# Performance work log

Hardware: AMD Instinct MI355X
Metric: run time of the kernel (lower is better)

## Reference

```python
import jax, jax.numpy as jnp
import numpy as np
from jax import lax

B, T, N, D, M, K, H = 16, 96, 256, 128, 1196, 8, 4
HD = D // H  # head dim = 32
TAU_TIME = 2.0


def setup_inputs() -> dict:
    key = jax.random.key(0)
    ks = jax.random.split(key, 12)
    w = lambda k, shp: jax.random.normal(k, shp, jnp.float32) * 0.05
    return {
        "x_scalar": jax.random.normal(ks[0], (B, T, N), jnp.float32),
        "season_q": jax.random.randint(ks[1], (B,), 0, 4),
        "year_q": 2010.0 + 10.0 * jax.random.uniform(ks[2], (B,), jnp.float32),
        "dw_w": w(ks[3], (N, 1, 12)),          # depthwise Conv1d weight (out=N, in/groups=1, k=12)
        "dw_b": jnp.zeros((N,), jnp.float32),
        "pw_w": w(ks[4], (N * D, N)),          # pointwise Conv1d weight (out=N*D, in=N), k=1 squeezed
        "pw_b": jnp.zeros((N * D,), jnp.float32),
        "ln_g": jnp.ones((D,), jnp.float32),
        "ln_b": jnp.zeros((D,), jnp.float32),
        "memory_bank": jax.random.normal(ks[5], (M, N, D), jnp.float32),
        "memory_seasons": jax.random.randint(ks[6], (M,), 0, 4),
        "memory_years": 2010.0 + 10.0 * jax.random.uniform(ks[7], (M,), jnp.float32),
        "in_proj_w": w(ks[8], (3 * D, D)),     # MHA packed q/k/v projection
        "in_proj_b": jnp.zeros((3 * D,), jnp.float32),
        "out_proj_w": w(ks[9], (D, D)),
        "out_proj_b": jnp.zeros((D,), jnp.float32),
        "proj_w": w(ks[10], (D, D)),
        "proj_b": jnp.zeros((D,), jnp.float32),
    }


def _layernorm(x, g, b, eps=1e-5):
    mu = jnp.mean(x, axis=-1, keepdims=True)
    var = jnp.mean((x - mu) ** 2, axis=-1, keepdims=True)
    return (x - mu) * lax.rsqrt(var + eps) * g + b


def _l2norm(x, eps=1e-12):
    n = jnp.sqrt(jnp.sum(x * x, axis=-1, keepdims=True))
    return x / jnp.maximum(n, eps)


def _forward(x_scalar, season_q, year_q, dw_w, dw_b, pw_w, pw_b, ln_g, ln_b,
             memory_bank, memory_seasons, memory_years,
             in_proj_w, in_proj_b, out_proj_w, out_proj_b, proj_w, proj_b):
    b, t, n = x_scalar.shape
    d = ln_g.shape[0]
    m = memory_bank.shape[0]

    # --- TemporalEncoder ---
    x = jnp.transpose(x_scalar, (0, 2, 1))  # (b, n, t): permute(0,2,3,1).reshape with d_input=1
    x = lax.conv_general_dilated(
        x, dw_w, window_strides=(1,), padding=[(6, 6)],
        dimension_numbers=("NCH", "OIH", "NCH"), feature_group_count=n)
    x = jax.nn.gelu(x + dw_b[:, None], approximate=False)      # (b, n, t+1)
    x = jnp.einsum("bct,oc->bot", x, pw_w) + pw_b[:, None]     # pointwise 1x1 conv -> (b, n*d, t+1)
    x = jax.nn.gelu(x, approximate=False)
    x = jnp.mean(x, axis=-1).reshape(b, n, d)                  # adaptive avg pool to 1
    q = _layernorm(x, ln_g, ln_b)                              # (b, n, d)

    # --- retrieve ---
    qf = _l2norm(q.reshape(b, n * d))
    memf = _l2norm(memory_bank.reshape(m, n * d))
    sim = qf @ memf.T                                          # (b, m)
    smask = (season_q[:, None] == memory_seasons[None, :]).astype(sim.dtype)
    sim = sim * smask + (1.0 - smask) * (-10000.0)
    dy = jnp.abs(year_q[:, None] - memory_years[None, :])
    diversity = 1.0 - jnp.exp(-dy / max(TAU_TIME, 1e-4))
    sim = sim * (0.5 + 0.5 * diversity)
    _, idx = lax.top_k(sim, K)                                 # (b, K)
    retrieved = memory_bank[idx]                               # (b, K, n, d)

    # --- cross attention: query (b*n, 1, d) vs kv (b*n, K, d) ---
    Wq, Wk, Wv = in_proj_w[:d], in_proj_w[d:2 * d], in_proj_w[2 * d:]
    bq, bk, bv = in_proj_b[:d], in_proj_b[d:2 * d], in_proj_b[2 * d:]
    kv = jnp.transpose(retrieved, (0, 2, 1, 3))                # (b, n, K, d)
    qp = (jnp.einsum("bnd,ed->bne", q, Wq) + bq).reshape(b, n, H, HD)
    kp = (jnp.einsum("bnkd,ed->bnke", kv, Wk) + bk).reshape(b, n, K, H, HD)
    vp = (jnp.einsum("bnkd,ed->bnke", kv, Wv) + bv).reshape(b, n, K, H, HD)
    scores = jnp.einsum("bnhe,bnkhe->bnhk", qp, kp) / np.sqrt(HD)
    attn = jax.nn.softmax(scores, axis=-1)
    ctx = jnp.einsum("bnhk,bnkhe->bnhe", attn, vp).reshape(b, n, d)
    out = jnp.einsum("bnd,ed->bne", ctx, out_proj_w) + out_proj_b
    out = jnp.einsum("bnd,ed->bne", out, proj_w) + proj_b
    return out, q


def reference(x_scalar, season_q, year_q, dw_w, dw_b, pw_w, pw_b, ln_g, ln_b,
              memory_bank, memory_seasons, memory_years,
              in_proj_w, in_proj_b, out_proj_w, out_proj_b, proj_w, proj_b):
    return _forward(x_scalar, season_q, year_q, dw_w, dw_b, pw_w, pw_b, ln_g, ln_b,
                    memory_bank, memory_seasons, memory_years,
                    in_proj_w, in_proj_b, out_proj_w, out_proj_b, proj_w, proj_b)
```

## Files before the change

kernel.cpp:

```cpp
#include <hip/hip_runtime.h>

typedef _Float16 f16x8 __attribute__((ext_vector_type(8)));
typedef _Float16 f16x4 __attribute__((ext_vector_type(4)));
typedef float    f32x4 __attribute__((ext_vector_type(4)));

__device__ __forceinline__ float gelu_f(float x) {
    float z  = 0.70710678118654752440f * x;
    float az = fabsf(z);
    float t  = 1.0f / fmaf(0.3275911f, az, 1.0f);
    float e  = __expf(-az * az);
    float p  = t * fmaf(t, fmaf(t, fmaf(t, fmaf(t, 1.061405429f, -1.453152027f),
                                        1.421413741f), -0.284496736f), 0.254829592f);
    float er = fmaf(-p, e, 1.0f);
    float s  = (z < 0.0f) ? -er : er;
    return 0.5f * x * (1.0f + s);
}

__device__ __forceinline__ void gload16(const void* g, void* l) {
    __builtin_amdgcn_global_load_lds(
        (const __attribute__((address_space(1))) unsigned int*)g,
        (__attribute__((address_space(3))) unsigned int*)l, 16, 0, 0);
}

__global__ void conv_kernel(const float* __restrict__ xs, const float* __restrict__ dww,
                            const float* __restrict__ dwb, _Float16* __restrict__ Gt)
{
    int b = blockIdx.x, t = blockIdx.y, n = threadIdx.x;
    float g = 0.f;
    if (t < 97) {
        float y = 0.f;
        #pragma unroll
        for (int j = 0; j < 12; ++j) {
            int tt = t + j - 6;
            if (tt >= 0 && tt < 96)
                y += dww[n*12 + j] * xs[((size_t)b*96 + tt)*256 + n];
        }
        g = gelu_f(y + dwb[n]);
    }
    Gt[((size_t)b*128 + t)*256 + n] = (_Float16)g;
}

__global__ void cvt_pw_kernel(const float* __restrict__ src, _Float16* __restrict__ dst,
                              const float* __restrict__ ipw, const float* __restrict__ opw,
                              const float* __restrict__ pjw, _Float16* __restrict__ wAll,
                              float* __restrict__ zp)
{
    int bid = blockIdx.x, tid = threadIdx.x;
    if (bid < 8192) {
        size_t i = ((size_t)bid*256 + tid) * 4;
        float4 v = *(const float4*)&src[i];
        f16x4 o; o[0] = (_Float16)v.x; o[1] = (_Float16)v.y; o[2] = (_Float16)v.z; o[3] = (_Float16)v.w;
        *(f16x4*)&dst[i] = o;
    } else if (bid < 8512) {
        int i = (bid - 8192)*256 + tid;
        float v = (i < 49152) ? ipw[i] : (i < 65536 ? opw[i - 49152] : pjw[i - 65536]);
        wAll[i] = (_Float16)v;
    } else {
        int i = (bid - 8512)*256 + tid;
        if (i < 5087) {
            float4 z = {0.f, 0.f, 0.f, 0.f};
            *(float4*)&zp[i*4] = z;
        }
    }
}

__global__ __launch_bounds__(256) void pw_kernel(const _Float16* __restrict__ W,
                                                 const _Float16* __restrict__ Gt,
                                                 const float* __restrict__ pwb,
                                                 float* __restrict__ xmean)
{
    __shared__ __align__(16) _Float16 As[2][128][32];
    __shared__ __align__(16) _Float16 Bs[2][128][32];

    int x = blockIdx.x;
    int xcd = x & 7, ii = x >> 3;
    int ob = xcd * 32 + (ii >> 4);
    int b  = ii & 15;
    const _Float16* Arow = W  + (size_t)ob * 128 * 256;
    const _Float16* Brow = Gt + (size_t)b  * 128 * 256;

    int tid = threadIdx.x, w = tid >> 6, l = tid & 63, lr = l & 15, lk = l >> 4;
    int wr = w >> 1, wc = w & 1;
    int rsw = (lr >> 1) & 3;

    f32x4 acc[4][4];
    #pragma unroll
    for (int i = 0; i < 4; ++i)
        #pragma unroll
        for (int j = 0; j < 4; ++j)
            acc[i][j] = f32x4{0.f, 0.f, 0.f, 0.f};

    auto stage = [&](int buf, int k0) {
        #pragma unroll
        for (int j = 0; j < 2; ++j) {
            int chunk = tid + j*256;
            int row = chunk >> 2;
            int co  = (chunk & 3) * 8;
            int cos = ((chunk & 3) ^ ((chunk >> 3) & 3)) * 8;
            gload16(&Arow[row*256 + k0 + cos], &As[buf][row][co]);
            gload16(&Brow[row*256 + k0 + cos], &Bs[buf][row][co]);
        }
    };

    stage(0, 0);
    __syncthreads();
    for (int ks = 0; ks < 8; ++ks) {
        int cur = ks & 1;
        if (ks < 7) stage(cur ^ 1, (ks + 1) * 32);
        f16x8 a[4], bb[4];
        #pragma unroll
        for (int i = 0; i < 4; ++i)
            a[i]  = *(const f16x8*)&As[cur][wr*64 + i*16 + lr][(lk ^ rsw)*8];
        #pragma unroll
        for (int j = 0; j < 4; ++j)
            if (wc == 0 || j < 3)
                bb[j] = *(const f16x8*)&Bs[cur][wc*64 + j*16 + lr][(lk ^ rsw)*8];
        #pragma unroll
        for (int i = 0; i < 4; ++i)
            #pragma unroll
            for (int j = 0; j < 4; ++j)
                if (wc == 0 || j < 3)
                    acc[i][j] = __builtin_amdgcn_mfma_f32_16x16x32_f16(bb[j], a[i], acc[i][j], 0, 0, 0);
        __syncthreads();
    }

    float (*red)[2] = reinterpret_cast<float(*)[2]>(&As[0][0][0]);
    #pragma unroll
    for (int i = 0; i < 4; ++i) {
        int og = ob*128 + wr*64 + i*16 + lr;
        float pbv = pwb[og];
        float s = 0.f;
        if (wc == 0) {
            #pragma unroll
            for (int j = 0; j < 4; ++j)
                #pragma unroll
                for (int r = 0; r < 4; ++r)
                    s += gelu_f(acc[i][j][r] + pbv);
        } else {
            #pragma unroll
            for (int j = 0; j < 2; ++j)
                #pragma unroll
                for (int r = 0; r < 4; ++r)
                    s += gelu_f(acc[i][j][r] + pbv);
            if (lk == 0) s += gelu_f(acc[i][2][0] + pbv);
        }
        s += __shfl_xor(s, 16, 64);
        s += __shfl_xor(s, 32, 64);
        if (lk == 0) red[wr*64 + i*16 + lr][wc] = s;
    }
    __syncthreads();
    if (tid < 128) {
        float v = (red[tid][0] + red[tid][1]) * (1.f / 97.f);
        xmean[(size_t)b*32768 + ob*128 + tid] = v;
    }
}

__global__ void ln_kernel(const float* __restrict__ xm, const float* __restrict__ g,
                          const float* __restrict__ bta, float* __restrict__ qout,
                          _Float16* __restrict__ qh, _Float16* __restrict__ qlo,
                          float* __restrict__ qss)
{
    int bn = blockIdx.x, lane = threadIdx.x;
    float x0 = xm[(size_t)bn*128 + lane];
    float x1 = xm[(size_t)bn*128 + 64 + lane];
    float s = x0 + x1;
    #pragma unroll
    for (int m = 1; m < 64; m <<= 1) s += __shfl_xor(s, m, 64);
    float mu = s * (1.f/128.f);
    float d0 = x0 - mu, d1 = x1 - mu;
    float v = d0*d0 + d1*d1;
    #pragma unroll
    for (int m = 1; m < 64; m <<= 1) v += __shfl_xor(v, m, 64);
    float rs = 1.0f / sqrtf(v * (1.f/128.f) + 1e-5f);
    float q0 = d0*rs*g[lane]    + bta[lane];
    float q1 = d1*rs*g[64+lane] + bta[64+lane];
    qout[(size_t)bn*128 + lane]      = q0;
    qout[(size_t)bn*128 + 64 + lane] = q1;
    _Float16 h0 = (_Float16)q0, h1 = (_Float16)q1;
    qh[(size_t)bn*128 + lane]      = h0;
    qh[(size_t)bn*128 + 64 + lane] = h1;
    qlo[(size_t)bn*128 + lane]      = (_Float16)(q0 - (float)h0);
    qlo[(size_t)bn*128 + 64 + lane] = (_Float16)(q1 - (float)h1);
    float ss = q0*q0 + q1*q1;
    #pragma unroll
    for (int m = 1; m < 64; m <<= 1) ss += __shfl_xor(ss, m, 64);
    if (lane == 0) atomicAdd(&qss[bn >> 8], ss);
}

__global__ __launch_bounds__(256) void simgemm_kernel(const _Float16* __restrict__ qhi,
                                                      const _Float16* __restrict__ qlo,
                                                      const float* __restrict__ mem,
                                                      float* __restrict__ dotp,
                                                      float* __restrict__ mn2)
{
    __shared__ __align__(16) float Ms[2][16][256];
    __shared__ f32x4 redls[4][64];
    __shared__ float redn[4][16];

    int tid = threadIdx.x, w = tid >> 6, l = tid & 63, lr = l & 15, lk = l >> 4;
    int m0 = blockIdx.y * 16;
    int kwin = blockIdx.x * 1024;
    int rowm = m0 + lr;

    auto stage = [&](int buf, int sw) {
        #pragma unroll
        for (int j = 0; j < 4; ++j) {
            int r = w*4 + j;
            int rowg = m0 + r; if (rowg > 1195) rowg = 1195;
            const float* src = mem + (size_t)rowg*32768 + kwin + sw*256 + (l ^ (r & 7))*4;
            gload16(src, &Ms[buf][r][0]);
        }
    };

    f32x4 acc_a = {0.f,0.f,0.f,0.f}, acc_b = {0.f,0.f,0.f,0.f};
    float nacc = 0.f;

    stage(0, 0);
    __syncthreads();
    for (int sw = 0; sw < 4; ++sw) {
        int cur = sw & 1;
        if (sw < 3) stage(cur ^ 1, sw + 1);
        #pragma unroll
        for (int cc = 0; cc < 2; ++cc) {
            int kl = w*64 + cc*32;
            int s0 = (kl + lk*8) >> 2;
            float4 v0 = *(const float4*)&Ms[cur][lr][(s0       ^ (lr & 7))*4];
            float4 v1 = *(const float4*)&Ms[cur][lr][((s0 + 1) ^ (lr & 7))*4];
            int kg = kwin + sw*256 + kl + lk*8;
            f16x8 ah = *(const f16x8*)&qhi[(size_t)lr*32768 + kg];
            f16x8 al = *(const f16x8*)&qlo[(size_t)lr*32768 + kg];
            float e0 = v0.x, e1 = v0.y, e2 = v0.z, e3 = v0.w;
            float e4 = v1.x, e5 = v1.y, e6 = v1.z, e7 = v1.w;
            f16x8 bh;
            bh[0]=(_Float16)e0; bh[1]=(_Float16)e1; bh[2]=(_Float16)e2; bh[3]=(_Float16)e3;
            bh[4]=(_Float16)e4; bh[5]=(_Float16)e5; bh[6]=(_Float16)e6; bh[7]=(_Float16)e7;
            nacc = fmaf(e0,e0, fmaf(e1,e1, fmaf(e2,e2, fmaf(e3,e3, nacc))));
            nacc = fmaf(e4,e4, fmaf(e5,e5, fmaf(e6,e6, fmaf(e7,e7, nacc))));
            acc_a = __builtin_amdgcn_mfma_f32_16x16x32_f16(ah, bh, acc_a, 0, 0, 0);
            acc_b = __builtin_amdgcn_mfma_f32_16x16x32_f16(al, bh, acc_b, 0, 0, 0);
        }
        __syncthreads();
    }

    nacc += __shfl_xor(nacc, 16, 64);
    nacc += __shfl_xor(nacc, 32, 64);

    f32x4 tot = acc_a + acc_b;
    redls[w][l] = tot;
    if (lk == 0) redn[w][lr] = nacc;
    __syncthreads();
    if (w == 0) {
        tot = redls[0][l];
        tot += redls[1][l]; tot += redls[2][l]; tot += redls[3][l];
        if (rowm < 1196) {
            #pragma unroll
            for (int r = 0; r < 4; ++r)
                atomicAdd(&dotp[(lk*4 + r)*1196 + rowm], tot[r]);
            if (lk == 0)
                atomicAdd(&mn2[rowm], redn[0][lr] + redn[1][lr] + redn[2][lr] + redn[3][lr]);
        }
    }
}

__global__ void topk_kernel(const float* __restrict__ dotp, const float* __restrict__ mn2,
                            const float* __restrict__ qss, const int* __restrict__ seaq,
                            const float* __restrict__ yq, const int* __restrict__ seam,
                            const float* __restrict__ ym, int* __restrict__ idx)
{
    __shared__ float sc[1216];
    int b = blockIdx.x, lane = threadIdx.x;
    float qn = fmaxf(sqrtf(qss[b]), 1e-12f);
    int sq = seaq[b];
    float yqv = yq[b];
    for (int m = lane; m < 1216; m += 64) {
        float v = -3e38f;
        if (m < 1196) {
            float s = dotp[b*1196 + m] / (qn * fmaxf(sqrtf(mn2[m]), 1e-12f));
            if (seam[m] != sq) s = -10000.0f;
            float dy = fabsf(yqv - ym[m]);
            v = s * (1.0f - 0.5f * expf(-0.5f * dy));
        }
        sc[m] = v;
    }
    __syncthreads();
    for (int kk = 0; kk < 8; ++kk) {
        float bv = -3e38f; int bi = 0x7fffffff;
        for (int m = lane; m < 1216; m += 64) {
            float v = sc[m];
            if (v > bv) { bv = v; bi = m; }
        }
        #pragma unroll
        for (int mk = 1; mk < 64; mk <<= 1) {
            float ov = __shfl_xor(bv, mk, 64);
            int   oi = __shfl_xor(bi, mk, 64);
            if (ov > bv || (ov == bv && oi < bi)) { bv = ov; bi = oi; }
        }
        if (lane == 0) { idx[b*8 + kk] = bi; sc[bi] = -3e38f; }
        __syncthreads();
    }
}

__global__ __launch_bounds__(256) void qkv_kernel(const _Float16* __restrict__ qh,
                                                  const float* __restrict__ memb,
                                                  const int* __restrict__ idx,
                                                  const _Float16* __restrict__ wAll,
                                                  const float* __restrict__ ipb,
                                                  _Float16* __restrict__ qp,
                                                  _Float16* __restrict__ kp,
                                                  _Float16* __restrict__ vp)
{
    int bid = blockIdx.x;
    const _Float16* Wm; const float* bias; _Float16* Y; int blk; int kv;
    if (bid < 64)       { kv = 0; Wm = wAll;         bias = ipb;       Y = qp; blk = bid; }
    else if (bid < 576) { kv = 1; Wm = wAll + 16384; bias = ipb + 128; Y = kp; blk = bid - 64; }
    else                { kv = 1; Wm = wAll + 32768; bias = ipb + 256; Y = vp; blk = bid - 576; }

    int tid = threadIdx.x, w = tid >> 6, l = tid & 63, lr = l & 15, lk = l >> 4;
    int r0 = blk * 64 + w * 16;

    const float* Af = nullptr;
    const _Float16* Ah = nullptr;
    if (kv) {
        int bk = (blk * 64) >> 8;
        int row = idx[bk];
        Af = memb + (size_t)row*32768 + ((r0 & 255) + lr)*128 + lk*8;
    } else {
        Ah = qh + (size_t)(r0 + lr)*128 + lk*8;
    }

    f32x4 acc[8];
    #pragma unroll
    for (int j = 0; j < 8; ++j) acc[j] = f32x4{0.f, 0.f, 0.f, 0.f};
    #pragma unroll
    for (int k0 = 0; k0 < 128; k0 += 32) {
        f16x8 a;
        if (kv) {
            float4 v0 = *(const float4*)&Af[k0];
            float4 v1 = *(const float4*)&Af[k0 + 4];
            a[0]=(_Float16)v0.x; a[1]=(_Float16)v0.y; a[2]=(_Float16)v0.z; a[3]=(_Float16)v0.w;
            a[4]=(_Float16)v1.x; a[5]=(_Float16)v1.y; a[6]=(_Float16)v1.z; a[7]=(_Float16)v1.w;
        } else {
            a = *(const f16x8*)&Ah[k0];
        }
        #pragma unroll
        for (int j = 0; j < 8; ++j) {
            f16x8 bb = *(const f16x8*)&Wm[(j*16 + lr)*128 + k0 + lk*8];
            acc[j] = __builtin_amdgcn_mfma_f32_16x16x32_f16(a, bb, acc[j], 0, 0, 0);
        }
    }
    #pragma unroll
    for (int j = 0; j < 8; ++j) {
        #pragma unroll
        for (int r = 0; r < 4; ++r) {
            int row = r0 + lk*4 + r, col = j*16 + lr;
            Y[(size_t)row*128 + col] = (_Float16)(acc[j][r] + bias[col]);
        }
    }
}

template<int OUT_F32>
__global__ __launch_bounds__(256) void gemm128_kernel(const _Float16* __restrict__ A,
                                                      const _Float16* __restrict__ W,
                                                      const float* __restrict__ bias,
                                                      void* __restrict__ Y, int R)
{
    int tid = threadIdx.x, w = tid >> 6, l = tid & 63, lr = l & 15, lk = l >> 4;
    int r0 = blockIdx.x * 64 + w * 16;
    f32x4 acc[8];
    #pragma unroll
    for (int j = 0; j < 8; ++j) acc[j] = f32x4{0.f, 0.f, 0.f, 0.f};
    #pragma unroll
    for (int k0 = 0; k0 < 128; k0 += 32) {
        f16x8 a = *(const f16x8*)&A[(size_t)(r0 + lr)*128 + k0 + lk*8];
        #pragma unroll
        for (int j = 0; j < 8; ++j) {
            f16x8 bb = *(const f16x8*)&W[(j*16 + lr)*128 + k0 + lk*8];
            acc[j] = __builtin_amdgcn_mfma_f32_16x16x32_f16(a, bb, acc[j], 0, 0, 0);
        }
    }
    #pragma unroll
    for (int j = 0; j < 8; ++j) {
        #pragma unroll
        for (int r = 0; r < 4; ++r) {
            int row = r0 + lk*4 + r, col = j*16 + lr;
            float v = acc[j][r] + bias[col];
            if (OUT_F32) ((float*)Y)[(size_t)row*128 + col] = v;
            else         ((_Float16*)Y)[(size_t)row*128 + col] = (_Float16)v;
        }
    }
}

__global__ void attn_kernel(const _Float16* __restrict__ qp, const _Float16* __restrict__ kp,
                            const _Float16* __restrict__ vp, _Float16* __restrict__ ctx)
{
    int bn = blockIdx.x;
    int b = bn >> 8, n = bn & 255;
    int tid = threadIdx.x;
    float qv = (float)qp[(size_t)bn*128 + tid];
    float sc[8];
    #pragma unroll
    for (int k = 0; k < 8; ++k) {
        float p = qv * (float)kp[(((size_t)(b*8 + k)*256 + n)*128) + tid];
        #pragma unroll
        for (int m = 1; m < 32; m <<= 1) p += __shfl_xor(p, m, 64);
        sc[k] = p * 0.17677669529663687f;
    }
    float mx = sc[0];
    #pragma unroll
    for (int k = 1; k < 8; ++k) mx = fmaxf(mx, sc[k]);
    float den = 0.f;
    #pragma unroll
    for (int k = 0; k < 8; ++k) { sc[k] = expf(sc[k] - mx); den += sc[k]; }
    float inv = 1.f / den;
    float c = 0.f;
    #pragma unroll
    for (int k = 0; k < 8; ++k)
        c += sc[k] * (float)vp[(((size_t)(b*8 + k)*256 + n)*128) + tid];
    ctx[(size_t)bn*128 + tid] = (_Float16)(c * inv);
}

extern "C" void kernel_launch(void* const* d_in, const int* in_sizes, int n_in,
                              void* d_out, int out_size, void* d_ws, size_t ws_size,
                              hipStream_t stream)
{
    const float* x_scalar = (const float*)d_in[0];
    const int*   season_q = (const int*)d_in[1];
    const float* year_q   = (const float*)d_in[2];
    const float* dw_w     = (const float*)d_in[3];
    const float* dw_b     = (const float*)d_in[4];
    const float* pw_w     = (const float*)d_in[5];
    const float* pw_b     = (const float*)d_in[6];
    const float* ln_g     = (const float*)d_in[7];
    const float* ln_b     = (const float*)d_in[8];
    const float* memb     = (const float*)d_in[9];
    const int*   mseas    = (const int*)d_in[10];
    const float* myear    = (const float*)d_in[11];
    const float* ipw      = (const float*)d_in[12];
    const float* ipb      = (const float*)d_in[13];
    const float* opw      = (const float*)d_in[14];
    const float* opb      = (const float*)d_in[15];
    const float* pjw      = (const float*)d_in[16];
    const float* pjb      = (const float*)d_in[17];

    char* wsb = (char*)d_ws;
    _Float16* Wf   = (_Float16*)(wsb + 0);
    _Float16* Gt   = (_Float16*)(wsb + 16777216);
    float*    xmean= (float*)   (wsb + 17825792);
    _Float16* qh   = (_Float16*)(wsb + 19922944);
    float*    qss  = (float*)   (wsb + 20971520);
    float*    dotp = (float*)   (wsb + 20971584);
    float*    mn2  = (float*)   (wsb + 21048128);
    int*      idxb = (int*)     (wsb + 21052928);
    _Float16* qp   = (_Float16*)(wsb + 29442048);
    _Float16* kp   = (_Float16*)(wsb + 30490624);
    _Float16* vp   = (_Float16*)(wsb + 38879232);
    _Float16* ctx  = (_Float16*)(wsb + 47267840);
    _Float16* out1 = (_Float16*)(wsb + 48316416);
    _Float16* wAll = (_Float16*)(wsb + 49364992);
    _Float16* qlo  = (_Float16*)(wsb + 49528832);

    float* outp = (float*)d_out;
    float* qout = (float*)d_out + 524288;

    cvt_pw_kernel<<<8532, 256, 0, stream>>>(pw_w, Wf, ipw, opw, pjw, wAll,
                                            (float*)(wsb + 20971520));
    conv_kernel<<<dim3(16, 128), 256, 0, stream>>>(x_scalar, dw_w, dw_b, Gt);

    pw_kernel<<<4096, 256, 0, stream>>>(Wf, Gt, pw_b, xmean);

    ln_kernel<<<4096, 64, 0, stream>>>(xmean, ln_g, ln_b, qout, qh, qlo, qss);

    simgemm_kernel<<<dim3(32, 75), 256, 0, stream>>>(qh, qlo, memb, dotp, mn2);
    topk_kernel<<<16, 64, 0, stream>>>(dotp, mn2, qss, season_q, year_q, mseas, myear, idxb);

    qkv_kernel<<<1088, 256, 0, stream>>>(qh, memb, idxb, wAll, ipb, qp, kp, vp);

    attn_kernel<<<4096, 128, 0, stream>>>(qp, kp, vp, ctx);

    gemm128_kernel<0><<<64, 256, 0, stream>>>(ctx,  wAll + 49152, opb, (void*)out1, 4096);
    gemm128_kernel<1><<<64, 256, 0, stream>>>(out1, wAll + 65536, pjb, (void*)outp, 4096);
}
```

Baseline: 243.8 us.

## Fuse layernorm into pointwise GEMM and fold output projections into attention

Layernorm moves into the pw_kernel epilogue, where one block already owns a full 128-wide row, so the xmean round trip and the separate ln_kernel launch go away. out_proj and proj are pre-multiplied into one 128x128 matrix and bias inside the weight-conversion kernel. Attention then applies that combined projection per row with scalar FMAs from shared memory, which replaces two MFMA GEMM launches and the ctx/out1 buffers. In exchange, each attention thread reads a full weight row with scalar math instead of tensor cores, and precomputing the weight product adds extra blocks to the conversion kernel.

```diff
diff --git a/kernel.cpp b/kernel.cpp
--- a/kernel.cpp
+++ b/kernel.cpp
@@ -42,8 +42,10 @@
 
 __global__ void cvt_pw_kernel(const float* __restrict__ src, _Float16* __restrict__ dst,
                               const float* __restrict__ ipw, const float* __restrict__ opw,
-                              const float* __restrict__ pjw, _Float16* __restrict__ wAll,
-                              float* __restrict__ zp)
+                              const float* __restrict__ pjw, const float* __restrict__ opb,
+                              const float* __restrict__ pjb, _Float16* __restrict__ wAll,
+                              float* __restrict__ zp, _Float16* __restrict__ Wcf,
+                              float* __restrict__ bc)
 {
     int bid = blockIdx.x, tid = threadIdx.x;
     if (bid < 8192) {
@@ -55,19 +57,37 @@
         int i = (bid - 8192)*256 + tid;
         float v = (i < 49152) ? ipw[i] : (i < 65536 ? opw[i - 49152] : pjw[i - 65536]);
         wAll[i] = (_Float16)v;
-    } else {
+    } else if (bid < 8532) {
         int i = (bid - 8512)*256 + tid;
         if (i < 5087) {
             float4 z = {0.f, 0.f, 0.f, 0.f};
             *(float4*)&zp[i*4] = z;
         }
+    } else {
+        int e = (bid - 8532)*2 + (tid >> 7);
+        int c = tid & 127;
+        float acc = 0.f;
+        for (int d = 0; d < 128; ++d)
+            acc = fmaf(pjw[e*128 + d], opw[d*128 + c], acc);
+        Wcf[e*128 + c] = (_Float16)acc;
+        if (c == 0) {
+            float s = pjb[e];
+            for (int d = 0; d < 128; ++d)
+                s = fmaf(pjw[e*128 + d], opb[d], s);
+            bc[e] = s;
+        }
     }
 }
 
 __global__ __launch_bounds__(256) void pw_kernel(const _Float16* __restrict__ W,
                                                  const _Float16* __restrict__ Gt,
                                                  const float* __restrict__ pwb,
-                                                 float* __restrict__ xmean)
+                                                 const float* __restrict__ lng,
+                                                 const float* __restrict__ lnb,
+                                                 float* __restrict__ qout,
+                                                 _Float16* __restrict__ qh,
+                                                 _Float16* __restrict__ qlo,
+                                                 float* __restrict__ qss)
 {
     __shared__ __align__(16) _Float16 As[2][128][32];
     __shared__ __align__(16) _Float16 Bs[2][128][32];
@@ -149,42 +169,34 @@
         if (lk == 0) red[wr*64 + i*16 + lr][wc] = s;
     }
     __syncthreads();
-    if (tid < 128) {
-        float v = (red[tid][0] + red[tid][1]) * (1.f / 97.f);
-        xmean[(size_t)b*32768 + ob*128 + tid] = v;
-    }
-}
-
-__global__ void ln_kernel(const float* __restrict__ xm, const float* __restrict__ g,
-                          const float* __restrict__ bta, float* __restrict__ qout,
-                          _Float16* __restrict__ qh, _Float16* __restrict__ qlo,
-                          float* __restrict__ qss)
-{
-    int bn = blockIdx.x, lane = threadIdx.x;
-    float x0 = xm[(size_t)bn*128 + lane];
-    float x1 = xm[(size_t)bn*128 + 64 + lane];
-    float s = x0 + x1;
-    #pragma unroll
-    for (int m = 1; m < 64; m <<= 1) s += __shfl_xor(s, m, 64);
-    float mu = s * (1.f/128.f);
-    float d0 = x0 - mu, d1 = x1 - mu;
-    float v = d0*d0 + d1*d1;
-    #pragma unroll
-    for (int m = 1; m < 64; m <<= 1) v += __shfl_xor(v, m, 64);
-    float rs = 1.0f / sqrtf(v * (1.f/128.f) + 1e-5f);
-    float q0 = d0*rs*g[lane]    + bta[lane];
-    float q1 = d1*rs*g[64+lane] + bta[64+lane];
-    qout[(size_t)bn*128 + lane]      = q0;
-    qout[(size_t)bn*128 + 64 + lane] = q1;
-    _Float16 h0 = (_Float16)q0, h1 = (_Float16)q1;
-    qh[(size_t)bn*128 + lane]      = h0;
-    qh[(size_t)bn*128 + 64 + lane] = h1;
-    qlo[(size_t)bn*128 + lane]      = (_Float16)(q0 - (float)h0);
-    qlo[(size_t)bn*128 + 64 + lane] = (_Float16)(q1 - (float)h1);
-    float ss = q0*q0 + q1*q1;
-    #pragma unroll
-    for (int m = 1; m < 64; m <<= 1) ss += __shfl_xor(ss, m, 64);
-    if (lane == 0) atomicAdd(&qss[bn >> 8], ss);
+
+    if (w == 0) {
+        float x0 = (red[l][0]      + red[l][1])      * (1.f/97.f);
+        float x1 = (red[64 + l][0] + red[64 + l][1]) * (1.f/97.f);
+        float sm = x0 + x1;
+        #pragma unroll
+        for (int m = 1; m < 64; m <<= 1) sm += __shfl_xor(sm, m, 64);
+        float mu = sm * (1.f/128.f);
+        float d0 = x0 - mu, d1 = x1 - mu;
+        float vv = d0*d0 + d1*d1;
+        #pragma unroll
+        for (int m = 1; m < 64; m <<= 1) vv += __shfl_xor(vv, m, 64);
+        float rs = 1.0f / sqrtf(vv * (1.f/128.f) + 1e-5f);
+        float q0 = d0*rs*lng[l]      + lnb[l];
+        float q1 = d1*rs*lng[64 + l] + lnb[64 + l];
+        size_t bn = (size_t)b*256 + ob;
+        qout[bn*128 + l]      = q0;
+        qout[bn*128 + 64 + l] = q1;
+        _Float16 h0 = (_Float16)q0, h1 = (_Float16)q1;
+        qh[bn*128 + l]       = h0;
+        qh[bn*128 + 64 + l]  = h1;
+        qlo[bn*128 + l]      = (_Float16)(q0 - (float)h0);
+        qlo[bn*128 + 64 + l] = (_Float16)(q1 - (float)h1);
+        float ss = q0*q0 + q1*q1;
+        #pragma unroll
+        for (int m = 1; m < 64; m <<= 1) ss += __shfl_xor(ss, m, 64);
+        if (l == 0) atomicAdd(&qss[b], ss);
+    }
 }
 
 __global__ __launch_bounds__(256) void simgemm_kernel(const _Float16* __restrict__ qhi,
@@ -358,41 +370,11 @@
     }
 }
 
-template<int OUT_F32>
-__global__ __launch_bounds__(256) void gemm128_kernel(const _Float16* __restrict__ A,
-                                                      const _Float16* __restrict__ W,
-                                                      const float* __restrict__ bias,
-                                                      void* __restrict__ Y, int R)
-{
-    int tid = threadIdx.x, w = tid >> 6, l = tid & 63, lr = l & 15, lk = l >> 4;
-    int r0 = blockIdx.x * 64 + w * 16;
-    f32x4 acc[8];
-    #pragma unroll
-    for (int j = 0; j < 8; ++j) acc[j] = f32x4{0.f, 0.f, 0.f, 0.f};
-    #pragma unroll
-    for (int k0 = 0; k0 < 128; k0 += 32) {
-        f16x8 a = *(const f16x8*)&A[(size_t)(r0 + lr)*128 + k0 + lk*8];
-        #pragma unroll
-        for (int j = 0; j < 8; ++j) {
-            f16x8 bb = *(const f16x8*)&W[(j*16 + lr)*128 + k0 + lk*8];
-            acc[j] = __builtin_amdgcn_mfma_f32_16x16x32_f16(a, bb, acc[j], 0, 0, 0);
-        }
-    }
-    #pragma unroll
-    for (int j = 0; j < 8; ++j) {
-        #pragma unroll
-        for (int r = 0; r < 4; ++r) {
-            int row = r0 + lk*4 + r, col = j*16 + lr;
-            float v = acc[j][r] + bias[col];
-            if (OUT_F32) ((float*)Y)[(size_t)row*128 + col] = v;
-            else         ((_Float16*)Y)[(size_t)row*128 + col] = (_Float16)v;
-        }
-    }
-}
-
 __global__ void attn_kernel(const _Float16* __restrict__ qp, const _Float16* __restrict__ kp,
-                            const _Float16* __restrict__ vp, _Float16* __restrict__ ctx)
-{
+                            const _Float16* __restrict__ vp, const _Float16* __restrict__ Wc,
+                            const float* __restrict__ bc, float* __restrict__ outp)
+{
+    __shared__ float ctxs[128];
     int bn = blockIdx.x;
     int b = bn >> 8, n = bn & 255;
     int tid = threadIdx.x;
@@ -416,7 +398,19 @@
     #pragma unroll
     for (int k = 0; k < 8; ++k)
         c += sc[k] * (float)vp[(((size_t)(b*8 + k)*256 + n)*128) + tid];
-    ctx[(size_t)bn*128 + tid] = (_Float16)(c * inv);
+    ctxs[tid] = c * inv;
+    __syncthreads();
+
+    float s = bc[tid];
+    const f16x8* wrow = (const f16x8*)&Wc[(size_t)tid*128];
+    #pragma unroll
+    for (int c0 = 0; c0 < 16; ++c0) {
+        f16x8 wv = wrow[c0];
+        #pragma unroll
+        for (int u = 0; u < 8; ++u)
+            s = fmaf(ctxs[c0*8 + u], (float)wv[u], s);
+    }
+    outp[(size_t)bn*128 + tid] = s;
 }
 
 extern "C" void kernel_launch(void* const* d_in, const int* in_sizes, int n_in,
@@ -445,8 +439,6 @@
     char* wsb = (char*)d_ws;
     _Float16* Wf   = (_Float16*)(wsb + 0);
     _Float16* Gt   = (_Float16*)(wsb + 16777216);
-    float*    xmean= (float*)   (wsb + 17825792);
-    _Float16* qh   = (_Float16*)(wsb + 19922944);
     float*    qss  = (float*)   (wsb + 20971520);
     float*    dotp = (float*)   (wsb + 20971584);
     float*    mn2  = (float*)   (wsb + 21048128);
@@ -454,29 +446,25 @@
     _Float16* qp   = (_Float16*)(wsb + 29442048);
     _Float16* kp   = (_Float16*)(wsb + 30490624);
     _Float16* vp   = (_Float16*)(wsb + 38879232);
-    _Float16* ctx  = (_Float16*)(wsb + 47267840);
-    _Float16* out1 = (_Float16*)(wsb + 48316416);
+    _Float16* Wcf  = (_Float16*)(wsb + 48316416);
+    float*    bc   = (float*)   (wsb + 48349184);
     _Float16* wAll = (_Float16*)(wsb + 49364992);
     _Float16* qlo  = (_Float16*)(wsb + 49528832);
+    _Float16* qh   = (_Float16*)(wsb + 19922944);
 
     float* outp = (float*)d_out;
     float* qout = (float*)d_out + 524288;
 
-    cvt_pw_kernel<<<8532, 256, 0, stream>>>(pw_w, Wf, ipw, opw, pjw, wAll,
-                                            (float*)(wsb + 20971520));
+    cvt_pw_kernel<<<8596, 256, 0, stream>>>(pw_w, Wf, ipw, opw, pjw, opb, pjb, wAll,
+                                            (float*)(wsb + 20971520), Wcf, bc);
     conv_kernel<<<dim3(16, 128), 256, 0, stream>>>(x_scalar, dw_w, dw_b, Gt);
 
-    pw_kernel<<<4096, 256, 0, stream>>>(Wf, Gt, pw_b, xmean);
-
-    ln_kernel<<<4096, 64, 0, stream>>>(xmean, ln_g, ln_b, qout, qh, qlo, qss);
+    pw_kernel<<<4096, 256, 0, stream>>>(Wf, Gt, pw_b, ln_g, ln_b, qout, qh, qlo, qss);
 
     simgemm_kernel<<<dim3(32, 75), 256, 0, stream>>>(qh, qlo, memb, dotp, mn2);
     topk_kernel<<<16, 64, 0, stream>>>(dotp, mn2, qss, season_q, year_q, mseas, myear, idxb);
 
     qkv_kernel<<<1088, 256, 0, stream>>>(qh, memb, idxb, wAll, ipb, qp, kp, vp);
 
-    attn_kernel<<<4096, 128, 0, stream>>>(qp, kp, vp, ctx);
-
-    gemm128_kernel<0><<<64, 256, 0, stream>>>(ctx,  wAll + 49152, opb, (void*)out1, 4096);
-    gemm128_kernel<1><<<64, 256, 0, stream>>>(out1, wAll + 65536, pjb, (void*)outp, 4096);
-}
+    attn_kernel<<<4096, 128, 0, stream>>>(qp, kp, vp, Wcf, bc, outp);
+}
```

Result: faster. 203.6 us (-16.5%).
